# Optimization experiments

Measured on AMD Instinct MI355X. Metric: run time of the kernel, lower is better.

The kernel has to match this reference:

```python
import jax, jax.numpy as jnp
import numpy as np

NEG = float(-2**32 + 1)  # padding value used by the original module
N_HEADS = 4


def setup_inputs() -> dict:
    key = jax.random.key(0)
    ks = jax.random.split(key, 12)
    B, L, H = 16, 200, 256
    queries = jax.random.normal(ks[0], (B, L, H), jnp.float32)
    keys = jax.random.normal(ks[1], (B, L, H), jnp.float32)
    time_mask = jax.random.randint(ks[2], (B, L), 0, 2) == 1
    attn_mask = jnp.triu(jnp.ones((L, L), dtype=bool), k=1)  # causal: True = masked
    time_matrix_K = jax.random.normal(ks[3], (B, L, L, H), jnp.float32) * 0.1
    time_matrix_V = jax.random.normal(ks[4], (B, L, L, H), jnp.float32) * 0.1
    abs_pos_K = jax.random.normal(ks[5], (B, L, H), jnp.float32)
    abs_pos_V = jax.random.normal(ks[6], (B, L, H), jnp.float32)
    s = 1.0 / np.sqrt(H)
    Wq = jax.random.normal(ks[7], (H, H), jnp.float32) * s
    Wk = jax.random.normal(ks[8], (H, H), jnp.float32) * s
    Wv = jax.random.normal(ks[9], (H, H), jnp.float32) * s
    bq = jnp.zeros((H,), jnp.float32)
    bk = jnp.zeros((H,), jnp.float32)
    bv = jnp.zeros((H,), jnp.float32)
    return dict(queries=queries, keys=keys, time_mask=time_mask, attn_mask=attn_mask,
                time_matrix_K=time_matrix_K, time_matrix_V=time_matrix_V,
                abs_pos_K=abs_pos_K, abs_pos_V=abs_pos_V,
                Wq=Wq, bq=bq, Wk=Wk, bk=bk, Wv=Wv, bv=bv)


def reference(queries, keys, time_mask, attn_mask, time_matrix_K, time_matrix_V,
              abs_pos_K, abs_pos_V, Wq, bq, Wk, bk, Wv, bv):
    B, L, H = queries.shape
    h = N_HEADS
    d = H // h
    # linear projections
    Q = (queries @ Wq.T + bq).reshape(B, L, h, d)
    K = (keys @ Wk.T + bk).reshape(B, L, h, d)
    V = (keys @ Wv.T + bv).reshape(B, L, h, d)
    posK = abs_pos_K.reshape(B, L, h, d)
    posV = abs_pos_V.reshape(B, L, h, d)
    tmK = time_matrix_K.reshape(B, L, L, h, d)
    tmV = time_matrix_V.reshape(B, L, L, h, d)
    # attention scores: content + absolute-position bias + per-row time bias
    scores = jnp.einsum('blhd,bmhd->bhlm', Q, K)
    scores += jnp.einsum('blhd,bmhd->bhlm', Q, posK)
    scores += jnp.einsum('blmhd,blhd->bhlm', tmK, Q)
    scores = scores / jnp.sqrt(jnp.asarray(d, scores.dtype))
    # time_mask masks query rows; attn_mask is causal [L,L]
    mask = time_mask[:, None, :, None] | attn_mask[None, None, :, :]  # [B,1,L,L]
    scores = jnp.where(mask, NEG, scores)
    A = jax.nn.softmax(scores, axis=-1)  # [B,h,L,L]; dropout_rate=0 -> identity
    out = jnp.einsum('bhlm,bmhd->blhd', A, V)
    out += jnp.einsum('bhlm,bmhd->blhd', A, posV)
    out += jnp.einsum('bhlm,blmhd->blhd', A, tmV)
    return out.reshape(B, L, H)
```

## Files before the change

kernel.cpp:

```cpp
#include <hip/hip_runtime.h>
#include <math.h>

#define LQ 200
#define HDIM 256

template <int CTRL>
__device__ __forceinline__ float dpp_add_step(float x) {
    int y = __builtin_amdgcn_update_dpp(0, __float_as_int(x), CTRL, 0xF, 0xF, true);
    return x + __int_as_float(y);
}
__device__ __forceinline__ float reduce16(float x) {
    x = dpp_add_step<0xB1>(x);
    x = dpp_add_step<0x4E>(x);
    x = dpp_add_step<0x141>(x);
    x = dpp_add_step<0x140>(x);
    return x;
}

__global__ __launch_bounds__(256) void proj_kernel(
    const float* __restrict__ queries, const float* __restrict__ keys,
    const float* __restrict__ posK, const float* __restrict__ posV,
    const float* __restrict__ Wq, const float* __restrict__ bq,
    const float* __restrict__ Wk, const float* __restrict__ bk,
    const float* __restrict__ Wv, const float* __restrict__ bv,
    float* __restrict__ Qp, float* __restrict__ Ksum, float* __restrict__ Vsum)
{
    __shared__ float qrow[8][HDIM];
    __shared__ float krow[8][HDIM];
    const int t = threadIdx.x;
    const int blk = blockIdx.x;
    const size_t base = (size_t)blk * 8 * HDIM;

    #pragma unroll
    for (int i = 0; i < 2; ++i) {
        int idx = i * 1024 + t * 4;
        *(float4*)&qrow[0][idx] = *(const float4*)&queries[base + idx];
        *(float4*)&krow[0][idx] = *(const float4*)&keys[base + idx];
    }
    __syncthreads();

    float accQ[8], accK[8], accV[8];
    #pragma unroll
    for (int r = 0; r < 8; ++r) { accQ[r] = 0.f; accK[r] = 0.f; accV[r] = 0.f; }

    const float4* wqp = (const float4*)&Wq[t * HDIM];
    const float4* wkp = (const float4*)&Wk[t * HDIM];
    const float4* wvp = (const float4*)&Wv[t * HDIM];

    for (int k4 = 0; k4 < HDIM / 4; ++k4) {
        float4 wq = wqp[k4], wk = wkp[k4], wv = wvp[k4];
        #pragma unroll
        for (int r = 0; r < 8; ++r) {
            float4 qv = *(const float4*)&qrow[r][k4 * 4];
            float4 kv = *(const float4*)&krow[r][k4 * 4];
            accQ[r] += qv.x * wq.x + qv.y * wq.y + qv.z * wq.z + qv.w * wq.w;
            accK[r] += kv.x * wk.x + kv.y * wk.y + kv.z * wk.z + kv.w * wk.w;
            accV[r] += kv.x * wv.x + kv.y * wv.y + kv.z * wv.z + kv.w * wv.w;
        }
    }

    const float bqv = bq[t], bkv = bk[t], bvv = bv[t];
    #pragma unroll
    for (int r = 0; r < 8; ++r) {
        size_t row = (size_t)blk * 8 + r;
        Qp[row * HDIM + t]   = (accQ[r] + bqv) * 0.125f;
        Ksum[row * HDIM + t] = accK[r] + bkv + posK[row * HDIM + t];
        Vsum[row * HDIM + t] = accV[r] + bvv + posV[row * HDIM + t];
    }
}

__global__ __launch_bounds__(256, 6) void attn_fused(
    const float* __restrict__ Qp, const float* __restrict__ Ksum,
    const float* __restrict__ Vsum, const float* __restrict__ tmK,
    const float* __restrict__ tmV, const int* __restrict__ tmask,
    float* __restrict__ out)
{
    __shared__ float outp[4][HDIM];
    __shared__ float Ssh[4][4];

    const int t = threadIdx.x;
    const int w = t >> 6;
    const int ln = t & 63;
    const int h = ln >> 4;
    const int c = ln * 4;
    const int blk = blockIdx.x;
    const int b = blk / LQ;
    const int l = blk - b * LQ;

    const bool rowmask = (tmask[blk] != 0);

    const float* pTV = tmV + (size_t)blk * (LQ * HDIM) + w * HDIM;
    const float* pVS = Vsum + (size_t)b * (LQ * HDIM) + w * HDIM;

    float4 acc = {0.f, 0.f, 0.f, 0.f};

    if (rowmask) {
        #pragma unroll 1
        for (int i = 0; i < LQ / 8; ++i) {
            const float4 a0 = *(const float4*)&pTV[c];
            const float4 b0 = *(const float4*)&pVS[c];
            const float4 a1 = *(const float4*)&pTV[4 * HDIM + c];
            const float4 b1 = *(const float4*)&pVS[4 * HDIM + c];
            acc.x += (a0.x + b0.x) + (a1.x + b1.x);
            acc.y += (a0.y + b0.y) + (a1.y + b1.y);
            acc.z += (a0.z + b0.z) + (a1.z + b1.z);
            acc.w += (a0.w + b0.w) + (a1.w + b1.w);
            pTV += 8 * HDIM;
            pVS += 8 * HDIM;
        }
        *(float4*)&outp[w][c] = acc;
        __syncthreads();
        out[(size_t)blk * HDIM + t] =
            (outp[0][t] + outp[1][t] + outp[2][t] + outp[3][t]) * (1.0f / LQ);
    } else {
        const float* pTK = tmK + (size_t)blk * (LQ * HDIM) + w * HDIM;
        const float* pKS = Ksum + (size_t)b * (LQ * HDIM) + w * HDIM;
        const float4 Q4 = *(const float4*)&Qp[(size_t)blk * HDIM + c];
        const int iters = (l >= w) ? ((l - w) >> 2) + 1 : 0;
        float S = 0.f;

        #pragma unroll 1
        for (int i = 0; i < iters; ++i) {
            const float4 k1 = *(const float4*)&pTK[c];
            const float4 k2 = *(const float4*)&pKS[c];
            const float4 v1 = *(const float4*)&pTV[c];
            const float4 v2 = *(const float4*)&pVS[c];
            float p = Q4.x * (k1.x + k2.x) + Q4.y * (k1.y + k2.y)
                    + Q4.z * (k1.z + k2.z) + Q4.w * (k1.w + k2.w);
            p = reduce16(p);
            const float e = __expf(p);
            acc.x += e * (v1.x + v2.x);
            acc.y += e * (v1.y + v2.y);
            acc.z += e * (v1.z + v2.z);
            acc.w += e * (v1.w + v2.w);
            S += e;
            pTK += 4 * HDIM;
            pKS += 4 * HDIM;
            pTV += 4 * HDIM;
            pVS += 4 * HDIM;
        }

        *(float4*)&outp[w][c] = acc;
        if ((ln & 15) == 0) Ssh[w][h] = S;
        __syncthreads();

        const int hh = t >> 6;
        const float Stot = Ssh[0][hh] + Ssh[1][hh] + Ssh[2][hh] + Ssh[3][hh];
        out[(size_t)blk * HDIM + t] =
            (outp[0][t] + outp[1][t] + outp[2][t] + outp[3][t]) / Stot;
    }
}

extern "C" void kernel_launch(void* const* d_in, const int* in_sizes, int n_in,
                              void* d_out, int out_size, void* d_ws, size_t ws_size,
                              hipStream_t stream) {
    const float* queries = (const float*)d_in[0];
    const float* keys    = (const float*)d_in[1];
    const int*   tmask   = (const int*)d_in[2];
    const float* tmK  = (const float*)d_in[4];
    const float* tmV  = (const float*)d_in[5];
    const float* posK = (const float*)d_in[6];
    const float* posV = (const float*)d_in[7];
    const float* Wq = (const float*)d_in[8];
    const float* bq = (const float*)d_in[9];
    const float* Wk = (const float*)d_in[10];
    const float* bk = (const float*)d_in[11];
    const float* Wv = (const float*)d_in[12];
    const float* bv = (const float*)d_in[13];

    float* ws   = (float*)d_ws;
    float* Qp   = ws;
    float* Ksum = ws + 819200;
    float* Vsum = ws + 2 * 819200;
    float* out  = (float*)d_out;

    hipLaunchKernelGGL(proj_kernel, dim3(400), dim3(256), 0, stream,
                       queries, keys, posK, posV, Wq, bq, Wk, bk, Wv, bv,
                       Qp, Ksum, Vsum);
    hipLaunchKernelGGL(attn_fused, dim3(3200), dim3(256), 0, stream,
                       Qp, Ksum, Vsum, tmK, tmV, tmask, out);
}
```

Before: 241.0 us.

## Software-pipeline attention loads, schedule longest causal rows first

Remaps block indices so the longest causal rows (largest l) launch first, interleaving batches, which evens out the load across the grid. Adds a 4-deep register prefetch ring in the causal loop so several rows' tmK/tmV loads are in flight while earlier rows are consumed. The masked-row path is unrolled by 8. Launch bounds are loosened from 6 to 4 waves to make room for the extra registers, which trades occupancy for memory-level parallelism.

```diff
diff --git a/kernel.cpp b/kernel.cpp
--- a/kernel.cpp
+++ b/kernel.cpp
@@ -69,7 +69,7 @@
     }
 }
 
-__global__ __launch_bounds__(256, 6) void attn_fused(
+__global__ __launch_bounds__(256, 4) void attn_fused(
     const float* __restrict__ Qp, const float* __restrict__ Ksum,
     const float* __restrict__ Vsum, const float* __restrict__ tmK,
     const float* __restrict__ tmV, const int* __restrict__ tmask,
@@ -83,62 +83,84 @@
     const int ln = t & 63;
     const int h = ln >> 4;
     const int c = ln * 4;
-    const int blk = blockIdx.x;
-    const int b = blk / LQ;
-    const int l = blk - b * LQ;
+    const int slot = blockIdx.x;
+    const int l = (LQ - 1) - (slot >> 4);
+    const int b = slot & 15;
+    const int blk = b * LQ + l;
 
     const bool rowmask = (tmask[blk] != 0);
 
-    const float* pTV = tmV + (size_t)blk * (LQ * HDIM) + w * HDIM;
-    const float* pVS = Vsum + (size_t)b * (LQ * HDIM) + w * HDIM;
+    const float* pTV = tmV + (size_t)blk * (LQ * HDIM) + w * HDIM + c;
+    const float* pVS = Vsum + (size_t)b * (LQ * HDIM) + w * HDIM + c;
 
     float4 acc = {0.f, 0.f, 0.f, 0.f};
 
     if (rowmask) {
-        #pragma unroll 1
-        for (int i = 0; i < LQ / 8; ++i) {
-            const float4 a0 = *(const float4*)&pTV[c];
-            const float4 b0 = *(const float4*)&pVS[c];
-            const float4 a1 = *(const float4*)&pTV[4 * HDIM + c];
-            const float4 b1 = *(const float4*)&pVS[4 * HDIM + c];
-            acc.x += (a0.x + b0.x) + (a1.x + b1.x);
-            acc.y += (a0.y + b0.y) + (a1.y + b1.y);
-            acc.z += (a0.z + b0.z) + (a1.z + b1.z);
-            acc.w += (a0.w + b0.w) + (a1.w + b1.w);
-            pTV += 8 * HDIM;
-            pVS += 8 * HDIM;
+        #pragma unroll 8
+        for (int i = 0; i < LQ / 4; ++i) {
+            const float4 a0 = *(const float4*)&pTV[(size_t)i * (4 * HDIM)];
+            const float4 b0 = *(const float4*)&pVS[(size_t)i * (4 * HDIM)];
+            acc.x += a0.x + b0.x;
+            acc.y += a0.y + b0.y;
+            acc.z += a0.z + b0.z;
+            acc.w += a0.w + b0.w;
         }
         *(float4*)&outp[w][c] = acc;
         __syncthreads();
         out[(size_t)blk * HDIM + t] =
             (outp[0][t] + outp[1][t] + outp[2][t] + outp[3][t]) * (1.0f / LQ);
     } else {
-        const float* pTK = tmK + (size_t)blk * (LQ * HDIM) + w * HDIM;
-        const float* pKS = Ksum + (size_t)b * (LQ * HDIM) + w * HDIM;
+        const float* pTK = tmK + (size_t)blk * (LQ * HDIM) + w * HDIM + c;
+        const float* pKS = Ksum + (size_t)b * (LQ * HDIM) + w * HDIM + c;
         const float4 Q4 = *(const float4*)&Qp[(size_t)blk * HDIM + c];
-        const int iters = (l >= w) ? ((l - w) >> 2) + 1 : 0;
+        const int n = (l >= w) ? ((l - w) >> 2) + 1 : 0;
         float S = 0.f;
 
-        #pragma unroll 1
-        for (int i = 0; i < iters; ++i) {
-            const float4 k1 = *(const float4*)&pTK[c];
-            const float4 k2 = *(const float4*)&pKS[c];
-            const float4 v1 = *(const float4*)&pTV[c];
-            const float4 v2 = *(const float4*)&pVS[c];
-            float p = Q4.x * (k1.x + k2.x) + Q4.y * (k1.y + k2.y)
-                    + Q4.z * (k1.z + k2.z) + Q4.w * (k1.w + k2.w);
-            p = reduce16(p);
-            const float e = __expf(p);
-            acc.x += e * (v1.x + v2.x);
-            acc.y += e * (v1.y + v2.y);
-            acc.z += e * (v1.z + v2.z);
-            acc.w += e * (v1.w + v2.w);
-            S += e;
-            pTK += 4 * HDIM;
-            pKS += 4 * HDIM;
-            pTV += 4 * HDIM;
-            pVS += 4 * HDIM;
+        float4 rk1_0, rk1_1, rk1_2, rk1_3;
+        float4 rk2_0, rk2_1, rk2_2, rk2_3;
+        float4 rv1_0, rv1_1, rv1_2, rv1_3;
+        float4 rv2_0, rv2_1, rv2_2, rv2_3;
+
+        #define LOADSLOT(SL, I) do {                                          \
+            rk1_##SL = *(const float4*)&pTK[(size_t)(I) * (4 * HDIM)];        \
+            rk2_##SL = *(const float4*)&pKS[(size_t)(I) * (4 * HDIM)];        \
+            rv1_##SL = *(const float4*)&pTV[(size_t)(I) * (4 * HDIM)];        \
+            rv2_##SL = *(const float4*)&pVS[(size_t)(I) * (4 * HDIM)];        \
+        } while (0)
+
+        #define CONSUME(SL) do {                                              \
+            float p = Q4.x * (rk1_##SL.x + rk2_##SL.x)                        \
+                    + Q4.y * (rk1_##SL.y + rk2_##SL.y)                        \
+                    + Q4.z * (rk1_##SL.z + rk2_##SL.z)                        \
+                    + Q4.w * (rk1_##SL.w + rk2_##SL.w);                       \
+            p = reduce16(p);                                                  \
+            const float e = __expf(p);                                        \
+            acc.x += e * (rv1_##SL.x + rv2_##SL.x);                           \
+            acc.y += e * (rv1_##SL.y + rv2_##SL.y);                           \
+            acc.z += e * (rv1_##SL.z + rv2_##SL.z);                           \
+            acc.w += e * (rv1_##SL.w + rv2_##SL.w);                           \
+            S += e;                                                           \
+        } while (0)
+
+        if (n > 0) LOADSLOT(0, 0);
+        if (n > 1) LOADSLOT(1, 1);
+        if (n > 2) LOADSLOT(2, 2);
+        if (n > 3) LOADSLOT(3, 3);
+
+        const int nfull = n & ~3;
+        for (int ib = 0; ib < nfull; ib += 4) {
+            CONSUME(0); if (ib + 4 < n) LOADSLOT(0, ib + 4);
+            CONSUME(1); if (ib + 5 < n) LOADSLOT(1, ib + 5);
+            CONSUME(2); if (ib + 6 < n) LOADSLOT(2, ib + 6);
+            CONSUME(3); if (ib + 7 < n) LOADSLOT(3, ib + 7);
         }
+        const int rem = n - nfull;
+        if (rem > 0) CONSUME(0);
+        if (rem > 1) CONSUME(1);
+        if (rem > 2) CONSUME(2);
+
+        #undef LOADSLOT
+        #undef CONSUME
 
         *(float4*)&outp[w][c] = acc;
         if ((ln & 15) == 0) Ssh[w][h] = S;
```

Measured after the change: 227.6 us, median of 2. -5.6%, faster.
